# Optimization experiments

Hardware: AMD Instinct MI355X
Metric: run time of the kernel (lower is better)

Reference implementation:

```python
import jax, jax.numpy as jnp
import numpy as np

N = 50000        # nodes
E = 800000       # edges
F_IN = 8         # node features per period
PERIODS = 12     # temporal periods
HID = 32         # A3TGCN2 out_channels
NTF = 2          # number_target_features
B = 2            # batch_size


def setup_inputs() -> dict:
    key = jax.random.key(0)
    ks = jax.random.split(key, 18)
    s = 0.1
    inp = {
        "x": jax.random.normal(ks[0], (B, N, F_IN, PERIODS), jnp.float32),
        "edge_index": jax.random.randint(ks[1], (2, E), 0, N, jnp.int32),
        "attention": jax.random.uniform(ks[2], (PERIODS,), jnp.float32),
        # GCNConv weights/biases for the 3 GRU gates (z, r, h)
        "Wz": jax.random.normal(ks[3], (F_IN, HID), jnp.float32) * s,
        "bz": jnp.zeros((HID,), jnp.float32),
        "Wr": jax.random.normal(ks[4], (F_IN, HID), jnp.float32) * s,
        "br": jnp.zeros((HID,), jnp.float32),
        "Wh": jax.random.normal(ks[5], (F_IN, HID), jnp.float32) * s,
        "bh": jnp.zeros((HID,), jnp.float32),
        # Linear(2*HID, HID) for each gate (stored as (in, out))
        "Lz": jax.random.normal(ks[6], (2 * HID, HID), jnp.float32) * s,
        "lbz": jnp.zeros((HID,), jnp.float32),
        "Lr": jax.random.normal(ks[7], (2 * HID, HID), jnp.float32) * s,
        "lbr": jnp.zeros((HID,), jnp.float32),
        "Lh": jax.random.normal(ks[8], (2 * HID, HID), jnp.float32) * s,
        "lbh": jnp.zeros((HID,), jnp.float32),
        # trailing Linear(32, periods * number_target_features)
        "Wout": jax.random.normal(ks[9], (HID, PERIODS * NTF), jnp.float32) * s,
        "bout": jnp.zeros((PERIODS * NTF,), jnp.float32),
    }
    return inp


def _gcn_prep(edge_index):
    # GCN normalization with added self-loops: D^{-1/2} (A+I) D^{-1/2}
    loops = jnp.arange(N, dtype=edge_index.dtype)
    src = jnp.concatenate([edge_index[0], loops])
    dst = jnp.concatenate([edge_index[1], loops])
    deg = jnp.zeros((N,), jnp.float32).at[dst].add(1.0)
    dinv = jnp.where(deg > 0, jax.lax.rsqrt(deg), 0.0)
    norm = dinv[src] * dinv[dst]
    return src, dst, norm


def _gcn(xp, W, b, src, dst, norm):
    # xp: (B, N, F) -> (B, N, HID); gather-scale-scatter per edge
    h = xp @ W
    msg = h[:, src, :] * norm[None, :, None]          # (B, E+N, HID)
    agg = jnp.zeros_like(h).at[:, dst, :].add(msg)    # scatter-add to targets
    return agg + b


def reference(x, edge_index, attention, Wz, bz, Wr, br, Wh, bh,
              Lz, lbz, Lr, lbr, Lh, lbh, Wout, bout):
    src, dst, norm = _gcn_prep(edge_index)
    probs = jax.nn.softmax(attention)                 # temporal attention
    xs = jnp.moveaxis(x, -1, 0)                       # (P, B, N, F)
    H0 = jnp.zeros((x.shape[0], x.shape[1], HID), x.dtype)

    def step(carry, inputs):
        H, acc = carry
        xp, p = inputs
        Z = jax.nn.sigmoid(
            jnp.concatenate([_gcn(xp, Wz, bz, src, dst, norm), H], -1) @ Lz + lbz)
        R = jax.nn.sigmoid(
            jnp.concatenate([_gcn(xp, Wr, br, src, dst, norm), H], -1) @ Lr + lbr)
        Ht = jnp.tanh(
            jnp.concatenate([_gcn(xp, Wh, bh, src, dst, norm), H * R], -1) @ Lh + lbh)
        Hn = Z * H + (1.0 - Z) * Ht                   # GRU update
        return (Hn, acc + p * Hn), None

    (_, H_accum), _ = jax.lax.scan(step, (H0, H0), (xs, probs))
    out = jax.nn.relu(H_accum) @ Wout + bout          # (B, N, P*NTF)
    return out.reshape(x.shape[0], x.shape[1], NTF, PERIODS)
```

## Files before the change

kernel.cpp:

```cpp
#include <hip/hip_runtime.h>


#define NN 50000
#define NE 800000
#define FIN 8
#define PER 12
#define HID 32
#define BATCH 2
#define FP 96
#define BN (BATCH * NN)
#define OUTF 24

#define OFF_PROBS  0
#define OFF_WPK    16
#define GSTRIDE    1312
#define OFF_WOUT   3952
#define OFF_BOUT   4720
#define SM_TOT     4744

#define OFF_DINV   4744
#define OFF_DEGI   54744
#define OFF_CURSOR 104744
#define OFF_ROWPTR 154744
#define OFF_COL    204752
#define OFF_WGT    1004752
#define OFF_AX     1804752
#define WS_FLOATS  11404752

__device__ __forceinline__ float fast_exp2(float x) {
#if __has_builtin(__builtin_amdgcn_exp2f)
    return __builtin_amdgcn_exp2f(x);
#else
    return exp2f(x);
#endif
}
__device__ __forceinline__ float fast_rcp(float x) {
#if __has_builtin(__builtin_amdgcn_rcpf)
    return __builtin_amdgcn_rcpf(x);
#else
    return 1.0f / x;
#endif
}
__device__ __forceinline__ float sigm(float x) {
    return fast_rcp(1.0f + fast_exp2(-1.4426950408889634f * x));
}
__device__ __forceinline__ float tanh_fast(float x) {
    return 2.0f * fast_rcp(1.0f + fast_exp2(-2.8853900817779268f * x)) - 1.0f;
}

__global__ void k_deg(const int* __restrict__ dst, int* __restrict__ degi) {
    int e = blockIdx.x * blockDim.x + threadIdx.x;
    if (e < NE) atomicAdd(&degi[dst[e]], 1);
}

__global__ void k_prep(const float* __restrict__ att,
                       const float* __restrict__ Wz, const float* __restrict__ bz,
                       const float* __restrict__ Wr, const float* __restrict__ br,
                       const float* __restrict__ Wh, const float* __restrict__ bh,
                       const float* __restrict__ Lz, const float* __restrict__ lbz,
                       const float* __restrict__ Lr, const float* __restrict__ lbr,
                       const float* __restrict__ Lh, const float* __restrict__ lbh,
                       const float* __restrict__ Wout, const float* __restrict__ bout,
                       float* __restrict__ ws) {
    int tid = threadIdx.x;
    if (tid == 0) {
        float a[PER], m = -1e30f, s = 0.0f;
        for (int i = 0; i < PER; i++) { a[i] = att[i]; m = fmaxf(m, a[i]); }
        for (int i = 0; i < PER; i++) { a[i] = __expf(a[i] - m); s += a[i]; }
        for (int i = 0; i < PER; i++) ws[OFF_PROBS + i] = a[i] / s;
    }
    int k = tid >> 5, j = tid & 31;
    const float* Ws[3]  = { Wz, Wr, Wh };
    const float* Ls[3]  = { Lz, Lr, Lh };
    const float* bs[3]  = { bz, br, bh };
    const float* lbs[3] = { lbz, lbr, lbh };
    for (int g = 0; g < 3; g++) {
        float* wp = ws + OFF_WPK + g * GSTRIDE;
        float acc = 0.0f;
        for (int i = 0; i < HID; i++) acc += Ws[g][k * HID + i] * Ls[g][i * HID + j];
        wp[k * HID + j] = acc;
        for (int i = tid; i < 1024; i += 256) wp[256 + i] = Ls[g][1024 + i];
        if (tid < HID) {
            float c = lbs[g][tid];
            for (int i = 0; i < HID; i++) c += bs[g][i] * Ls[g][i * HID + tid];
            wp[1280 + tid] = c;
        }
    }
    for (int i = tid; i < 768; i += 256) ws[OFF_WOUT + i] = Wout[i];
    if (tid < OUTF) ws[OFF_BOUT + tid] = bout[tid];
}

#define STRIP 49
__global__ __launch_bounds__(1024)
void k_scan(const int* __restrict__ degi, int* __restrict__ rowptr,
            float* __restrict__ dinv) {
    __shared__ int wsum[16];
    int tid = threadIdx.x;
    int lane = tid & 63, wid = tid >> 6;
    int s0 = tid * STRIP;
    int vals[STRIP];
    int sum = 0;
    #pragma unroll
    for (int i = 0; i < STRIP; i++) {
        int idx = s0 + i;
        int d = (idx < NN) ? degi[idx] : 0;
        vals[i] = d;
        sum += d;
        if (idx < NN) dinv[idx] = rsqrtf(1.0f + (float)d);
    }
    int run = sum;
    #pragma unroll
    for (int off = 1; off < 64; off <<= 1) {
        int t = __shfl_up(run, off);
        if (lane >= off) run += t;
    }
    if (lane == 63) wsum[wid] = run;
    __syncthreads();
    if (wid == 0 && lane < 16) {
        int v = wsum[lane];
        #pragma unroll
        for (int off = 1; off < 16; off <<= 1) {
            int t = __shfl_up(v, off);
            if (lane >= off) v += t;
        }
        wsum[lane] = v;
    }
    __syncthreads();
    int base = (wid ? wsum[wid - 1] : 0) + (run - sum);
    if (tid == 0) rowptr[0] = 0;
    #pragma unroll
    for (int i = 0; i < STRIP; i++) {
        int idx = s0 + i;
        if (idx < NN) { base += vals[i]; rowptr[idx + 1] = base; }
    }
}

__global__ void k_csr(const int* __restrict__ src, const int* __restrict__ dst,
                      const int* __restrict__ rowptr, int* __restrict__ cursor,
                      const float* __restrict__ dinv,
                      int* __restrict__ col, float* __restrict__ wgt) {
    int e = blockIdx.x * blockDim.x + threadIdx.x;
    if (e >= NE) return;
    int s = src[e], d = dst[e];
    int pos = atomicAdd(&cursor[d], 1);
    int i = rowptr[d] + pos;
    col[i] = s;
    wgt[i] = dinv[s] * dinv[d];
}

__global__ __launch_bounds__(256)
void k_agg(const float* __restrict__ x,
           const int* __restrict__ rowptr, const int* __restrict__ col,
           const float* __restrict__ wgt, const float* __restrict__ dinv,
           float* __restrict__ AX) {
    int n = blockIdx.x * blockDim.x + threadIdx.x;
    if (n >= NN) return;
    const float* xb = x + (size_t)blockIdx.y * (NN * FP);
    float* axb = AX + (size_t)blockIdx.y * NN + n;
    int r0 = rowptr[n], r1 = rowptr[n + 1];

    float4 acc[24];
    #pragma unroll
    for (int c = 0; c < 24; c++) acc[c] = make_float4(0.f, 0.f, 0.f, 0.f);

    #pragma unroll 1
    for (int i = r0; i < r1; i++) {
        int s = col[i];
        float w = wgt[i];
        const float* row = xb + (size_t)s * FP;
        float4 v[24];
        #pragma unroll
        for (int c = 0; c < 24; c++) v[c] = *(const float4*)(row + c * 4);
        __builtin_amdgcn_sched_barrier(0);
        #pragma unroll
        for (int c = 0; c < 24; c++) {
            acc[c].x = fmaf(w, v[c].x, acc[c].x);
            acc[c].y = fmaf(w, v[c].y, acc[c].y);
            acc[c].z = fmaf(w, v[c].z, acc[c].z);
            acc[c].w = fmaf(w, v[c].w, acc[c].w);
        }
    }
    {
        float di = dinv[n];
        float w = di * di;
        const float* row = xb + (size_t)n * FP;
        float4 v[24];
        #pragma unroll
        for (int c = 0; c < 24; c++) v[c] = *(const float4*)(row + c * 4);
        __builtin_amdgcn_sched_barrier(0);
        #pragma unroll
        for (int c = 0; c < 24; c++) {
            acc[c].x = fmaf(w, v[c].x, acc[c].x);
            acc[c].y = fmaf(w, v[c].y, acc[c].y);
            acc[c].z = fmaf(w, v[c].z, acc[c].z);
            acc[c].w = fmaf(w, v[c].w, acc[c].w);
        }
    }
    #pragma unroll
    for (int c = 0; c < 24; c++) {
        axb[(size_t)(4 * c + 0) * BN] = acc[c].x;
        axb[(size_t)(4 * c + 1) * BN] = acc[c].y;
        axb[(size_t)(4 * c + 2) * BN] = acc[c].z;
        axb[(size_t)(4 * c + 3) * BN] = acc[c].w;
    }
}


#define XCAT_(a,b) a##b
#define XCAT(a,b) XCAT_(a,b)

#define FOR32(OP) \
    OP(0,x,0)  OP(0,y,1)  OP(0,z,2)  OP(0,w,3) \
    OP(1,x,4)  OP(1,y,5)  OP(1,z,6)  OP(1,w,7) \
    OP(2,x,8)  OP(2,y,9)  OP(2,z,10) OP(2,w,11) \
    OP(3,x,12) OP(3,y,13) OP(3,z,14) OP(3,w,15) \
    OP(4,x,16) OP(4,y,17) OP(4,z,18) OP(4,w,19) \
    OP(5,x,20) OP(5,y,21) OP(5,z,22) OP(5,w,23) \
    OP(6,x,24) OP(6,y,25) OP(6,z,26) OP(6,w,27) \
    OP(7,x,28) OP(7,y,29) OP(7,z,30) OP(7,w,31)

#define FOR8AB(OP) \
    OP(0,x,0,ua,ub) OP(0,y,1,ub,ua) OP(0,z,2,ua,ub) OP(0,w,3,ub,ua) \
    OP(1,x,4,ua,ub) OP(1,y,5,ub,ua) OP(1,z,6,ua,ub) OP(1,w,7,ub,ua)

#define FOR32AB(OP) \
    OP(0,x,0,ua,ub)  OP(0,y,1,ub,ua)  OP(0,z,2,ua,ub)  OP(0,w,3,ub,ua) \
    OP(1,x,4,ua,ub)  OP(1,y,5,ub,ua)  OP(1,z,6,ua,ub)  OP(1,w,7,ub,ua) \
    OP(2,x,8,ua,ub)  OP(2,y,9,ub,ua)  OP(2,z,10,ua,ub) OP(2,w,11,ub,ua) \
    OP(3,x,12,ua,ub) OP(3,y,13,ub,ua) OP(3,z,14,ua,ub) OP(3,w,15,ub,ua) \
    OP(4,x,16,ua,ub) OP(4,y,17,ub,ua) OP(4,z,18,ua,ub) OP(4,w,19,ub,ua) \
    OP(5,x,20,ua,ub) OP(5,y,21,ub,ua) OP(5,z,22,ua,ub) OP(5,w,23,ub,ua) \
    OP(6,x,24,ua,ub) OP(6,y,25,ub,ua) OP(6,z,26,ua,ub) OP(6,w,27,ub,ua) \
    OP(7,x,28,ua,ub) OP(7,y,29,ub,ua) OP(7,z,30,ua,ub) OP(7,w,31,ub,ua)

#define FMA4(dd, ss, vv) \
    dd.x = fmaf((ss), (vv).x, dd.x); dd.y = fmaf((ss), (vv).y, dd.y); \
    dd.z = fmaf((ss), (vv).z, dd.z); dd.w = fmaf((ss), (vv).w, dd.w);

#define SBAR() __builtin_amdgcn_sched_barrier(0)

#define ROWLD(U, W, ofs) \
    XCAT(U,0) = *(const float4*)((W) + (ofs)); \
    XCAT(U,1) = *(const float4*)((W) + (ofs) + 4); \
    XCAT(U,2) = *(const float4*)((W) + (ofs) + 8); \
    XCAT(U,3) = *(const float4*)((W) + (ofs) + 12); \
    XCAT(U,4) = *(const float4*)((W) + (ofs) + 16); \
    XCAT(U,5) = *(const float4*)((W) + (ofs) + 20); \
    XCAT(U,6) = *(const float4*)((W) + (ofs) + 24); \
    XCAT(U,7) = *(const float4*)((W) + (ofs) + 28);

#define ROWFMA(P, a, U) do { \
    float av = (a); \
    FMA4(XCAT(P,0), av, XCAT(U,0)) FMA4(XCAT(P,1), av, XCAT(U,1)) \
    FMA4(XCAT(P,2), av, XCAT(U,2)) FMA4(XCAT(P,3), av, XCAT(U,3)) \
    FMA4(XCAT(P,4), av, XCAT(U,4)) FMA4(XCAT(P,5), av, XCAT(U,5)) \
    FMA4(XCAT(P,6), av, XCAT(U,6)) FMA4(XCAT(P,7), av, XCAT(U,7)) \
} while (0)

#define LDB(P, W) \
    XCAT(P,0) = *(const float4*)((W) + 1280); XCAT(P,1) = *(const float4*)((W) + 1284); \
    XCAT(P,2) = *(const float4*)((W) + 1288); XCAT(P,3) = *(const float4*)((W) + 1292); \
    XCAT(P,4) = *(const float4*)((W) + 1296); XCAT(P,5) = *(const float4*)((W) + 1300); \
    XCAT(P,6) = *(const float4*)((W) + 1304); XCAT(P,7) = *(const float4*)((W) + 1308);

#define GIN_STEP(i,c,n,CUR,NXT) \
    ROWLD(NXT, Wg, ((n) < 7 ? 32*((n)+1) : 256)); \
    ROWFMA(GP, XCAT(in,i).c, CUR); SBAR();

#define GH_STEP(i,c,n,CUR,NXT) \
    ROWLD(NXT, Wg, 256 + 32*((n) < 31 ? (n)+1 : 31)); \
    ROWFMA(GP, XCAT(GS,i).c, CUR); SBAR();

#define GATE_PIPE() \
    LDB(GP, Wg); ROWLD(ua, Wg, 0); SBAR(); \
    FOR8AB(GIN_STEP) \
    FOR32AB(GH_STEP)

#define ZERO_OP(i,c,n) h##i.c = 0.0f; ac##i.c = 0.0f;
#define HR_OP(i,c,n)   o##i.c = sigm(o##i.c) * h##i.c;
#define TANH_OP(i,c,n) t##i.c = tanh_fast(t##i.c);
#define UPD_OP(i,c,n)  { float Zv = sigm(o##i.c); \
                         h##i.c = fmaf(Zv, h##i.c - t##i.c, t##i.c); \
                         ac##i.c = fmaf(pp, h##i.c, ac##i.c); }

#define OROW(a, ofs) do { \
    float4 u0 = *(const float4*)(WO + (ofs)); \
    float4 u1 = *(const float4*)(WO + (ofs) + 4); \
    float4 u2 = *(const float4*)(WO + (ofs) + 8); \
    float4 u3 = *(const float4*)(WO + (ofs) + 12); \
    float4 u4 = *(const float4*)(WO + (ofs) + 16); \
    float4 u5 = *(const float4*)(WO + (ofs) + 20); \
    float av = (a); \
    FMA4(q0, av, u0) FMA4(q1, av, u1) FMA4(q2, av, u2) \
    FMA4(q3, av, u3) FMA4(q4, av, u4) FMA4(q5, av, u5) \
    SBAR(); \
} while (0)

#define OUT_OP(i,c,n) OROW(fmaxf(ac##i.c, 0.0f), (n) * OUTF);

__global__ __launch_bounds__(64)
void k_gru(const float* __restrict__ AX, const float* __restrict__ wp,
           float* __restrict__ out) {
    __shared__ __align__(16) float sm[SM_TOT];
    int tid = threadIdx.x;
    for (int i = tid; i < SM_TOT; i += 64) sm[i] = wp[i];
    __syncthreads();

    int g = blockIdx.x * 64 + tid;
    if (g >= BN) return;

    const float* WZ = sm + OFF_WPK;
    const float* WR = sm + OFF_WPK + GSTRIDE;
    const float* WH = sm + OFF_WPK + 2 * GSTRIDE;

    float4 h0, h1, h2, h3, h4, h5, h6, h7;
    float4 ac0, ac1, ac2, ac3, ac4, ac5, ac6, ac7;
    float4 o0, o1, o2, o3, o4, o5, o6, o7;
    float4 t0, t1, t2, t3, t4, t5, t6, t7;
    float4 ua0, ua1, ua2, ua3, ua4, ua5, ua6, ua7;
    float4 ub0, ub1, ub2, ub3, ub4, ub5, ub6, ub7;
    float4 in0, in1;
    FOR32(ZERO_OP)

    #pragma unroll 1
    for (int p = 0; p < PER; p++) {
        const float* axp = AX + (size_t)p * BN + g;
        in0.x = axp[0];
        in0.y = axp[(size_t)1 * PER * BN];
        in0.z = axp[(size_t)2 * PER * BN];
        in0.w = axp[(size_t)3 * PER * BN];
        in1.x = axp[(size_t)4 * PER * BN];
        in1.y = axp[(size_t)5 * PER * BN];
        in1.z = axp[(size_t)6 * PER * BN];
        in1.w = axp[(size_t)7 * PER * BN];
        float pp = sm[OFF_PROBS + p];

        #define GP o
        #define GS h
        { const float* Wg = WR; GATE_PIPE() }
        #undef GP
        #undef GS
        FOR32(HR_OP)

        #define GP t
        #define GS o
        { const float* Wg = WH; GATE_PIPE() }
        #undef GP
        #undef GS
        FOR32(TANH_OP)

        #define GP o
        #define GS h
        { const float* Wg = WZ; GATE_PIPE() }
        #undef GP
        #undef GS
        FOR32(UPD_OP)
    }

    const float* WO = sm + OFF_WOUT;
    const float* WB = sm + OFF_BOUT;
    float4 q0 = *(const float4*)(WB + 0);
    float4 q1 = *(const float4*)(WB + 4);
    float4 q2 = *(const float4*)(WB + 8);
    float4 q3 = *(const float4*)(WB + 12);
    float4 q4 = *(const float4*)(WB + 16);
    float4 q5 = *(const float4*)(WB + 20);
    FOR32(OUT_OP)

    float* op = out + (size_t)g * OUTF;
    *(float4*)(op + 0)  = q0; *(float4*)(op + 4)  = q1;
    *(float4*)(op + 8)  = q2; *(float4*)(op + 12) = q3;
    *(float4*)(op + 16) = q4; *(float4*)(op + 20) = q5;
}

extern "C" void kernel_launch(void* const* d_in, const int* in_sizes, int n_in,
                              void* d_out, int out_size, void* d_ws, size_t ws_size,
                              hipStream_t stream) {
    if (ws_size < (size_t)WS_FLOATS * sizeof(float)) return;

    const float* x    = (const float*)d_in[0];
    const int*   ei   = (const int*)d_in[1];
    const float* att  = (const float*)d_in[2];
    const float* Wz   = (const float*)d_in[3];
    const float* bz   = (const float*)d_in[4];
    const float* Wr   = (const float*)d_in[5];
    const float* br   = (const float*)d_in[6];
    const float* Wh   = (const float*)d_in[7];
    const float* bh   = (const float*)d_in[8];
    const float* Lz   = (const float*)d_in[9];
    const float* lbz  = (const float*)d_in[10];
    const float* Lr   = (const float*)d_in[11];
    const float* lbr  = (const float*)d_in[12];
    const float* Lh   = (const float*)d_in[13];
    const float* lbh  = (const float*)d_in[14];
    const float* Wout = (const float*)d_in[15];
    const float* bout = (const float*)d_in[16];
    float* out = (float*)d_out;
    float* ws  = (float*)d_ws;

    const int* src = ei;
    const int* dst = ei + NE;

    float* dinv   = ws + OFF_DINV;
    int*   degi   = (int*)(ws + OFF_DEGI);
    int*   cursor = (int*)(ws + OFF_CURSOR);
    int*   rowptr = (int*)(ws + OFF_ROWPTR);
    int*   col    = (int*)(ws + OFF_COL);
    float* wgt    = ws + OFF_WGT;
    float* AX     = ws + OFF_AX;

    hipMemsetAsync(degi, 0, 2 * (size_t)NN * sizeof(int), stream);
    k_deg<<<(NE + 255) / 256, 256, 0, stream>>>(dst, degi);
    k_prep<<<1, 256, 0, stream>>>(att, Wz, bz, Wr, br, Wh, bh,
                                  Lz, lbz, Lr, lbr, Lh, lbh, Wout, bout, ws);
    k_scan<<<1, 1024, 0, stream>>>(degi, rowptr, dinv);
    k_csr<<<(NE + 255) / 256, 256, 0, stream>>>(src, dst, rowptr, cursor, dinv, col, wgt);
    dim3 gAgg((NN + 255) / 256, 2);
    k_agg<<<gAgg, 256, 0, stream>>>(x, rowptr, col, wgt, dinv, AX);
    k_gru<<<(BN + 63) / 64, 64, 0, stream>>>(AX, ws, out);
}
```

Baseline: 546.0 us.

## Process both batch elements per thread in GRU kernel to reuse weight loads

Each thread of the GRU kernel now handles one node for both batch elements, so every shared-memory weight row it loads feeds two sets of FMAs. The grid is halved. This cuts LDS traffic per FLOP but roughly doubles the live register state (h, ac, o, t for two samples), which may spill or lower occupancy with only about 782 blocks of 64 threads.

```diff
diff --git a/kernel.cpp b/kernel.cpp
--- a/kernel.cpp
+++ b/kernel.cpp
@@ -265,23 +265,31 @@
 
 #define GIN_STEP(i,c,n,CUR,NXT) \
     ROWLD(NXT, Wg, ((n) < 7 ? 32*((n)+1) : 256)); \
-    ROWFMA(GP, XCAT(in,i).c, CUR); SBAR();
+    ROWFMA(GPA, XCAT(inA,i).c, CUR); \
+    ROWFMA(GPB, XCAT(inB,i).c, CUR); SBAR();
 
 #define GH_STEP(i,c,n,CUR,NXT) \
     ROWLD(NXT, Wg, 256 + 32*((n) < 31 ? (n)+1 : 31)); \
-    ROWFMA(GP, XCAT(GS,i).c, CUR); SBAR();
+    ROWFMA(GPA, XCAT(GSA,i).c, CUR); \
+    ROWFMA(GPB, XCAT(GSB,i).c, CUR); SBAR();
 
 #define GATE_PIPE() \
-    LDB(GP, Wg); ROWLD(ua, Wg, 0); SBAR(); \
+    LDB(GPA, Wg); LDB(GPB, Wg); ROWLD(ua, Wg, 0); SBAR(); \
     FOR8AB(GIN_STEP) \
     FOR32AB(GH_STEP)
 
-#define ZERO_OP(i,c,n) h##i.c = 0.0f; ac##i.c = 0.0f;
-#define HR_OP(i,c,n)   o##i.c = sigm(o##i.c) * h##i.c;
-#define TANH_OP(i,c,n) t##i.c = tanh_fast(t##i.c);
-#define UPD_OP(i,c,n)  { float Zv = sigm(o##i.c); \
-                         h##i.c = fmaf(Zv, h##i.c - t##i.c, t##i.c); \
-                         ac##i.c = fmaf(pp, h##i.c, ac##i.c); }
+#define ZERO_OP(i,c,n) hA##i.c = 0.0f; acA##i.c = 0.0f; \
+                       hB##i.c = 0.0f; acB##i.c = 0.0f;
+#define HR_OP(i,c,n)   oA##i.c = sigm(oA##i.c) * hA##i.c; \
+                       oB##i.c = sigm(oB##i.c) * hB##i.c;
+#define TANH_OP(i,c,n) tA##i.c = tanh_fast(tA##i.c); \
+                       tB##i.c = tanh_fast(tB##i.c);
+#define UPD_OP(i,c,n)  { float ZA = sigm(oA##i.c); \
+                         hA##i.c = fmaf(ZA, hA##i.c - tA##i.c, tA##i.c); \
+                         acA##i.c = fmaf(pp, hA##i.c, acA##i.c); \
+                         float ZB = sigm(oB##i.c); \
+                         hB##i.c = fmaf(ZB, hB##i.c - tB##i.c, tB##i.c); \
+                         acB##i.c = fmaf(pp, hB##i.c, acB##i.c); }
 
 #define OROW(a, ofs) do { \
     float4 u0 = *(const float4*)(WO + (ofs)); \
@@ -296,7 +304,8 @@
     SBAR(); \
 } while (0)
 
-#define OUT_OP(i,c,n) OROW(fmaxf(ac##i.c, 0.0f), (n) * OUTF);
+#define OUT_OP_A(i,c,n) OROW(fmaxf(acA##i.c, 0.0f), (n) * OUTF);
+#define OUT_OP_B(i,c,n) OROW(fmaxf(acB##i.c, 0.0f), (n) * OUTF);
 
 __global__ __launch_bounds__(64)
 void k_gru(const float* __restrict__ AX, const float* __restrict__ wp,
@@ -306,71 +315,106 @@
     for (int i = tid; i < SM_TOT; i += 64) sm[i] = wp[i];
     __syncthreads();
 
-    int g = blockIdx.x * 64 + tid;
-    if (g >= BN) return;
+    int n = blockIdx.x * 64 + tid;
+    if (n >= NN) return;
 
     const float* WZ = sm + OFF_WPK;
     const float* WR = sm + OFF_WPK + GSTRIDE;
     const float* WH = sm + OFF_WPK + 2 * GSTRIDE;
 
-    float4 h0, h1, h2, h3, h4, h5, h6, h7;
-    float4 ac0, ac1, ac2, ac3, ac4, ac5, ac6, ac7;
-    float4 o0, o1, o2, o3, o4, o5, o6, o7;
-    float4 t0, t1, t2, t3, t4, t5, t6, t7;
+    float4 hA0, hA1, hA2, hA3, hA4, hA5, hA6, hA7;
+    float4 hB0, hB1, hB2, hB3, hB4, hB5, hB6, hB7;
+    float4 acA0, acA1, acA2, acA3, acA4, acA5, acA6, acA7;
+    float4 acB0, acB1, acB2, acB3, acB4, acB5, acB6, acB7;
+    float4 oA0, oA1, oA2, oA3, oA4, oA5, oA6, oA7;
+    float4 oB0, oB1, oB2, oB3, oB4, oB5, oB6, oB7;
+    float4 tA0, tA1, tA2, tA3, tA4, tA5, tA6, tA7;
+    float4 tB0, tB1, tB2, tB3, tB4, tB5, tB6, tB7;
     float4 ua0, ua1, ua2, ua3, ua4, ua5, ua6, ua7;
     float4 ub0, ub1, ub2, ub3, ub4, ub5, ub6, ub7;
-    float4 in0, in1;
+    float4 inA0, inA1, inB0, inB1;
     FOR32(ZERO_OP)
 
     #pragma unroll 1
     for (int p = 0; p < PER; p++) {
-        const float* axp = AX + (size_t)p * BN + g;
-        in0.x = axp[0];
-        in0.y = axp[(size_t)1 * PER * BN];
-        in0.z = axp[(size_t)2 * PER * BN];
-        in0.w = axp[(size_t)3 * PER * BN];
-        in1.x = axp[(size_t)4 * PER * BN];
-        in1.y = axp[(size_t)5 * PER * BN];
-        in1.z = axp[(size_t)6 * PER * BN];
-        in1.w = axp[(size_t)7 * PER * BN];
+        const float* axp = AX + (size_t)p * BN + n;
+        inA0.x = axp[0];
+        inA0.y = axp[(size_t)1 * PER * BN];
+        inA0.z = axp[(size_t)2 * PER * BN];
+        inA0.w = axp[(size_t)3 * PER * BN];
+        inA1.x = axp[(size_t)4 * PER * BN];
+        inA1.y = axp[(size_t)5 * PER * BN];
+        inA1.z = axp[(size_t)6 * PER * BN];
+        inA1.w = axp[(size_t)7 * PER * BN];
+        inB0.x = axp[NN];
+        inB0.y = axp[(size_t)1 * PER * BN + NN];
+        inB0.z = axp[(size_t)2 * PER * BN + NN];
+        inB0.w = axp[(size_t)3 * PER * BN + NN];
+        inB1.x = axp[(size_t)4 * PER * BN + NN];
+        inB1.y = axp[(size_t)5 * PER * BN + NN];
+        inB1.z = axp[(size_t)6 * PER * BN + NN];
+        inB1.w = axp[(size_t)7 * PER * BN + NN];
         float pp = sm[OFF_PROBS + p];
 
-        #define GP o
-        #define GS h
+        #define GPA oA
+        #define GPB oB
+        #define GSA hA
+        #define GSB hB
         { const float* Wg = WR; GATE_PIPE() }
-        #undef GP
-        #undef GS
+        #undef GPA
+        #undef GPB
+        #undef GSA
+        #undef GSB
         FOR32(HR_OP)
 
-        #define GP t
-        #define GS o
+        #define GPA tA
+        #define GPB tB
+        #define GSA oA
+        #define GSB oB
         { const float* Wg = WH; GATE_PIPE() }
-        #undef GP
-        #undef GS
+        #undef GPA
+        #undef GPB
+        #undef GSA
+        #undef GSB
         FOR32(TANH_OP)
 
-        #define GP o
-        #define GS h
+        #define GPA oA
+        #define GPB oB
+        #define GSA hA
+        #define GSB hB
         { const float* Wg = WZ; GATE_PIPE() }
-        #undef GP
-        #undef GS
+        #undef GPA
+        #undef GPB
+        #undef GSA
+        #undef GSB
         FOR32(UPD_OP)
     }
 
     const float* WO = sm + OFF_WOUT;
     const float* WB = sm + OFF_BOUT;
-    float4 q0 = *(const float4*)(WB + 0);
-    float4 q1 = *(const float4*)(WB + 4);
-    float4 q2 = *(const float4*)(WB + 8);
-    float4 q3 = *(const float4*)(WB + 12);
-    float4 q4 = *(const float4*)(WB + 16);
-    float4 q5 = *(const float4*)(WB + 20);
-    FOR32(OUT_OP)
-
-    float* op = out + (size_t)g * OUTF;
-    *(float4*)(op + 0)  = q0; *(float4*)(op + 4)  = q1;
-    *(float4*)(op + 8)  = q2; *(float4*)(op + 12) = q3;
-    *(float4*)(op + 16) = q4; *(float4*)(op + 20) = q5;
+    float4 q0, q1, q2, q3, q4, q5;
+
+    q0 = *(const float4*)(WB + 0);  q1 = *(const float4*)(WB + 4);
+    q2 = *(const float4*)(WB + 8);  q3 = *(const float4*)(WB + 12);
+    q4 = *(const float4*)(WB + 16); q5 = *(const float4*)(WB + 20);
+    FOR32(OUT_OP_A)
+    {
+        float* op = out + (size_t)n * OUTF;
+        *(float4*)(op + 0)  = q0; *(float4*)(op + 4)  = q1;
+        *(float4*)(op + 8)  = q2; *(float4*)(op + 12) = q3;
+        *(float4*)(op + 16) = q4; *(float4*)(op + 20) = q5;
+    }
+
+    q0 = *(const float4*)(WB + 0);  q1 = *(const float4*)(WB + 4);
+    q2 = *(const float4*)(WB + 8);  q3 = *(const float4*)(WB + 12);
+    q4 = *(const float4*)(WB + 16); q5 = *(const float4*)(WB + 20);
+    FOR32(OUT_OP_B)
+    {
+        float* op = out + (size_t)(NN + n) * OUTF;
+        *(float4*)(op + 0)  = q0; *(float4*)(op + 4)  = q1;
+        *(float4*)(op + 8)  = q2; *(float4*)(op + 12) = q3;
+        *(float4*)(op + 16) = q4; *(float4*)(op + 20) = q5;
+    }
 }
 
 extern "C" void kernel_launch(void* const* d_in, const int* in_sizes, int n_in,
@@ -417,5 +461,5 @@
     k_csr<<<(NE + 255) / 256, 256, 0, stream>>>(src, dst, rowptr, cursor, dinv, col, wgt);
     dim3 gAgg((NN + 255) / 256, 2);
     k_agg<<<gAgg, 256, 0, stream>>>(x, rowptr, col, wgt, dinv, AX);
-    k_gru<<<(BN + 63) / 64, 64, 0, stream>>>(AX, ws, out);
-}
+    k_gru<<<(NN + 63) / 64, 64, 0, stream>>>(AX, ws, out);
+}
```

Result: slower. 597.5 us (+9.4%).
